# Kernel optimization log

Hardware: AMD Instinct MI355X
Metric: run time of the kernel (lower is better)

## Reference

```python
import jax, jax.numpy as jnp
import numpy as np

# dims
B, N, C_A, C_S, C_Z = 2, 8192, 128, 384, 16
H, D = 4, 32            # n_heads, head_dim (H*D == C_A)
NQ, NK = 32, 128        # local window: queries / keys
NB = 3                  # n_blocks
W = N // NQ             # number of query windows
HID = 2 * C_A           # transition expansion (n=2)


def _ln(x, eps=1e-5):
    # LayerNorm without affine params
    m = jnp.mean(x, axis=-1, keepdims=True)
    v = jnp.var(x, axis=-1, keepdims=True)
    return (x - m) * jax.lax.rsqrt(v + eps)


def setup_inputs() -> dict:
    key = jax.random.key(0)
    ks = iter(jax.random.split(key, 40))
    def rn(shape, scale=1.0):
        return jax.random.normal(next(ks), shape, dtype=jnp.float32) * jnp.float32(scale)
    inp = {
        'q': rn((B, N, C_A)),
        's': rn((B, N, C_S)),
        'p': rn((B, W, NQ, NK, C_Z)),
        # AttentionPairBias (AF3 Alg 24) params, stacked over blocks
        'adaln_scale_w': rn((NB, C_S, C_A), C_S ** -0.5),
        'adaln_scale_b': jnp.zeros((NB, C_A), jnp.float32),
        'adaln_shift_w': rn((NB, C_S, C_A), C_S ** -0.5),
        'wq': rn((NB, C_A, H * D), C_A ** -0.5),
        'bq': jnp.zeros((NB, H * D), jnp.float32),
        'wk': rn((NB, C_A, H * D), C_A ** -0.5),
        'wv': rn((NB, C_A, H * D), C_A ** -0.5),
        'lnz_w': jnp.ones((NB, C_Z), jnp.float32),
        'lnz_b': jnp.zeros((NB, C_Z), jnp.float32),
        'wb_pair': rn((NB, C_Z, H), C_Z ** -0.5),
        'wg': rn((NB, C_A, H * D), C_A ** -0.5),
        'wo': rn((NB, H * D, C_A), (H * D) ** -0.5),
        'sgate_w': rn((NB, C_S, C_A), C_S ** -0.5),
        'sgate_b': jnp.full((NB, C_A), -2.0, jnp.float32),
        # ConditionedTransitionBlock (AF3 Alg 25) params
        't_scale_w': rn((NB, C_S, C_A), C_S ** -0.5),
        't_scale_b': jnp.zeros((NB, C_A), jnp.float32),
        't_shift_w': rn((NB, C_S, C_A), C_S ** -0.5),
        't_wa': rn((NB, C_A, HID), C_A ** -0.5),
        't_wb': rn((NB, C_A, HID), C_A ** -0.5),
        't_wo': rn((NB, HID, C_A), HID ** -0.5),
        't_sgate_w': rn((NB, C_S, C_A), C_S ** -0.5),
        't_sgate_b': jnp.full((NB, C_A), -2.0, jnp.float32),
    }
    return inp


def reference(q, s, p,
              adaln_scale_w, adaln_scale_b, adaln_shift_w,
              wq, bq, wk, wv, lnz_w, lnz_b, wb_pair, wg, wo, sgate_w, sgate_b,
              t_scale_w, t_scale_b, t_shift_w, t_wa, t_wb, t_wo, t_sgate_w, t_sgate_b):
    a = q
    s_ln = _ln(s)  # [B, N, C_S], shared across blocks
    # local window key indices: window w covers queries [w*NQ, (w+1)*NQ), keys
    # are a centered NK-wide window -> offsets in [-(NK-NQ)//2, ...)
    off = (NK - NQ) // 2
    idx = jnp.arange(W)[:, None] * NQ - off + jnp.arange(NK)[None, :]  # [W, NK]
    valid = (idx >= 0) & (idx < N)
    idx_c = jnp.clip(idx, 0, N - 1)
    inv_sqrt_d = jnp.float32(1.0 / np.sqrt(D))
    NEG = jnp.float32(-1e9)

    for i in range(NB):
        # ---- AttentionPairBias (AdaLN-conditioned, pair-biased, gated) ----
        a_ln = _ln(a)
        a_ln = jax.nn.sigmoid(s_ln @ adaln_scale_w[i] + adaln_scale_b[i]) * a_ln \
               + s_ln @ adaln_shift_w[i]
        qh = (a_ln @ wq[i] + bq[i]).reshape(B, N, H, D)
        kh = (a_ln @ wk[i]).reshape(B, N, H, D)
        vh = (a_ln @ wv[i]).reshape(B, N, H, D)
        g = jax.nn.sigmoid(a_ln @ wg[i]).reshape(B, N, H, D)
        # pair bias from z: LN + linear to heads -> [B, W, NQ, NK, H]
        bias = (_ln(p) * lnz_w[i] + lnz_b[i]) @ wb_pair[i]
        qw = qh.reshape(B, W, NQ, H, D)
        kw = kh[:, idx_c]  # [B, W, NK, H, D]
        vw = vh[:, idx_c]
        logits = jnp.einsum('bwqhd,bwkhd->bwqkh', qw, kw) * inv_sqrt_d + bias
        logits = jnp.where(valid[None, :, None, :, None], logits, NEG)
        attn = jax.nn.softmax(logits, axis=3)
        ow = jnp.einsum('bwqkh,bwkhd->bwqhd', attn, vw)
        o = (g * ow.reshape(B, N, H, D)).reshape(B, N, H * D)
        attn_out = (o @ wo[i]) * jax.nn.sigmoid(s_ln @ sgate_w[i] + sgate_b[i])
        # ---- ConditionedTransitionBlock (SwiGLU, sigmoid-gated) ----
        t_ln = _ln(a)
        t_ln = jax.nn.sigmoid(s_ln @ t_scale_w[i] + t_scale_b[i]) * t_ln \
               + s_ln @ t_shift_w[i]
        hidden = jax.nn.silu(t_ln @ t_wa[i]) * (t_ln @ t_wb[i])
        trans_out = (hidden @ t_wo[i]) * jax.nn.sigmoid(s_ln @ t_sgate_w[i] + t_sgate_b[i])
        # AF3 Alg 23: a <- b + ConditionedTransitionBlock(a, s)
        a = attn_out + trans_out
    return a
```

## Files before the change

kernel.cpp:

```cpp
#include <hip/hip_runtime.h>
#include <hip/hip_bf16.h>
#include <cstddef>
#include <cstdint>

#define BB   2
#define NN   8192
#define CA   128
#define CS   384
#define CZ   16
#define HH   4
#define DD   32
#define NQW  32
#define NKW  128
#define NBLK 3
#define WW   256
#define MR   (BB*NN)
#define HIDN 256

typedef unsigned short u16;
typedef __attribute__((ext_vector_type(8))) short short8;
typedef __attribute__((ext_vector_type(4))) float floatx4;

__device__ __forceinline__ float sigmoidf_(float x) { return 1.f / (1.f + __expf(-x)); }

__device__ __forceinline__ u16 f2bf(float x) {
  unsigned u = __float_as_uint(x);
  unsigned r = (u + 0x7fffu + ((u >> 16) & 1u)) >> 16;
  return (u16)r;
}
__device__ __forceinline__ float bf2f(u16 u) {
  return __uint_as_float(((unsigned)u) << 16);
}

__device__ __forceinline__ void gload16(const u16* g, u16* l) {
  __builtin_amdgcn_global_load_lds(
      (const __attribute__((address_space(1))) unsigned int*)g,
      (__attribute__((address_space(3))) unsigned int*)l, 16, 0, 0);
}

__global__ __launch_bounds__(256) void ln_s_kernel(const float* __restrict__ s,
                                                   u16* __restrict__ s_ln_bf) {
  int row  = blockIdx.x * 4 + (threadIdx.x >> 6);
  int lane = threadIdx.x & 63;
  const float* sr = s + (size_t)row * CS;
  float x[6];
  float sum = 0.f, sq = 0.f;
#pragma unroll
  for (int t = 0; t < 6; ++t) { x[t] = sr[lane + 64*t]; sum += x[t]; sq += x[t]*x[t]; }
#pragma unroll
  for (int off = 32; off; off >>= 1) { sum += __shfl_down(sum, off); sq += __shfl_down(sq, off); }
  sum = __shfl(sum, 0); sq = __shfl(sq, 0);
  float mean = sum * (1.f/CS);
  float var  = sq  * (1.f/CS) - mean*mean;
  float rstd = rsqrtf(var + 1e-5f);
  u16* orow = s_ln_bf + (size_t)row * CS;
#pragma unroll
  for (int t = 0; t < 6; ++t) orow[lane + 64*t] = f2bf((x[t]-mean)*rstd);
}

__global__ __launch_bounds__(256) void modln_kernel(const float* __restrict__ a,
                                                    const u16* __restrict__ sp0,
                                                    const u16* __restrict__ sp1,
                                                    const u16* __restrict__ sp3,
                                                    const u16* __restrict__ sp4,
                                                    u16* __restrict__ amod,
                                                    u16* __restrict__ tmod) {
  int row  = blockIdx.x * 4 + (threadIdx.x >> 6);
  int lane = threadIdx.x & 63;
  const float* ar = a + (size_t)row * CA;
  float x0 = ar[lane], x1 = ar[lane + 64];
  float sum = x0 + x1, sq = x0*x0 + x1*x1;
#pragma unroll
  for (int off = 32; off; off >>= 1) { sum += __shfl_down(sum, off); sq += __shfl_down(sq, off); }
  sum = __shfl(sum, 0); sq = __shfl(sq, 0);
  float mean = sum * (1.f/CA);
  float var  = sq  * (1.f/CA) - mean*mean;
  float rstd = rsqrtf(var + 1e-5f);
  float n0 = (x0-mean)*rstd, n1 = (x1-mean)*rstd;
  size_t i0 = (size_t)row * CA + lane;
  amod[i0]      = f2bf(bf2f(sp0[i0])     *n0 + bf2f(sp1[i0]));
  amod[i0 + 64] = f2bf(bf2f(sp0[i0 + 64])*n1 + bf2f(sp1[i0 + 64]));
  tmod[i0]      = f2bf(bf2f(sp3[i0])     *n0 + bf2f(sp4[i0]));
  tmod[i0 + 64] = f2bf(bf2f(sp3[i0 + 64])*n1 + bf2f(sp4[i0 + 64]));
}

struct TJob { const float* src; u16* dst; int K; int N; };
struct TJobs { TJob j[42]; };

__global__ __launch_bounds__(256) void transpose_bf16(TJobs jobs) {
  TJob jb = jobs.j[blockIdx.z];
  int tk = blockIdx.x * 32, tn = blockIdx.y * 32;
  if (tk >= jb.K || tn >= jb.N) return;
  __shared__ float tile[32][33];
  int tx = threadIdx.x & 31;
  int ty = threadIdx.x >> 5;
#pragma unroll
  for (int r = ty; r < 32; r += 8) tile[r][tx] = jb.src[(size_t)(tk + r) * jb.N + tn + tx];
  __syncthreads();
#pragma unroll
  for (int r = ty; r < 32; r += 8)
    jb.dst[(size_t)(tn + r) * jb.K + tk + tx] = f2bf(tile[tx][r]);
}

struct GemmJob {
  const u16* A;
  const u16* Bt;
  const u16* Bt2;
  const float* bias;
  u16* outbf;
  int K;
  int ostride;
  int mode;
  int pad;
};
struct GemmJobs { GemmJob j[18]; };

template <int J, bool DUAL>
__global__ __launch_bounds__(256) void gemm_mfma(GemmJobs jobs) {
  const int jbase = blockIdx.z * J;
  const GemmJob jb0 = jobs.j[jbase];
  const int bm = blockIdx.y * 128, bn = blockIdx.x * 128;
  const int K = jb0.K;

  __shared__ u16 As[2][4096];
  __shared__ u16 Bs[2][J][4096];
  __shared__ u16 Bs2[DUAL ? 2 : 1][DUAL ? 4096 : 8];

  const int tid  = threadIdx.x;
  const int lane = tid & 63;
  const int wave = tid >> 6;
  const int wr = wave >> 1, wc = wave & 1;
  const int l15 = lane & 15, quad = lane >> 4;

  floatx4 acc[J][4][4] = {};
  floatx4 acc2[DUAL ? 4 : 1][DUAL ? 4 : 1] = {};

  const u16* Ab0 = jb0.A + ((size_t)bm + lane) * K + wave * 8;
  const u16* Ab1 = jb0.A + ((size_t)bm + 64 + lane) * K + wave * 8;
  const u16* Bb0[J];
  const u16* Bb1[J];
#pragma unroll
  for (int jj = 0; jj < J; ++jj) {
    const u16* Bt = jobs.j[jbase + jj].Bt;
    Bb0[jj] = Bt + ((size_t)bn + lane) * K + wave * 8;
    Bb1[jj] = Bt + ((size_t)bn + 64 + lane) * K + wave * 8;
  }
  const u16* B2b0 = DUAL ? (jb0.Bt2 + ((size_t)bn + lane) * K + wave * 8) : nullptr;
  const u16* B2b1 = DUAL ? (jb0.Bt2 + ((size_t)bn + 64 + lane) * K + wave * 8) : nullptr;

  auto stage = [&](int k0, int pb) {
    gload16(Ab0 + k0, As[pb] + wave * 1024);
    gload16(Ab1 + k0, As[pb] + wave * 1024 + 512);
#pragma unroll
    for (int jj = 0; jj < J; ++jj) {
      gload16(Bb0[jj] + k0, Bs[pb][jj] + wave * 1024);
      gload16(Bb1[jj] + k0, Bs[pb][jj] + wave * 1024 + 512);
    }
    if constexpr (DUAL) {
      gload16(B2b0 + k0, Bs2[pb] + wave * 1024);
      gload16(B2b1 + k0, Bs2[pb] + wave * 1024 + 512);
    }
  };

  stage(0, 0);
  __syncthreads();
  int cur = 0;
  for (int k0 = 0; k0 < K; k0 += 32) {
    if (k0 + 32 < K) stage(k0 + 32, cur ^ 1);

    short8 a_frag[4];
#pragma unroll
    for (int mt = 0; mt < 4; ++mt)
      a_frag[mt] = *(const short8*)(As[cur] + quad * 1024 + (wr * 64 + mt * 16 + l15) * 8);
#pragma unroll
    for (int jj = 0; jj < J; ++jj) {
      short8 b_frag[4];
#pragma unroll
      for (int nt = 0; nt < 4; ++nt)
        b_frag[nt] = *(const short8*)(Bs[cur][jj] + quad * 1024 + (wc * 64 + nt * 16 + l15) * 8);
#pragma unroll
      for (int mt = 0; mt < 4; ++mt)
#pragma unroll
        for (int nt = 0; nt < 4; ++nt)
          acc[jj][mt][nt] = __builtin_amdgcn_mfma_f32_16x16x32_bf16(a_frag[mt], b_frag[nt], acc[jj][mt][nt], 0, 0, 0);
    }
    if constexpr (DUAL) {
      short8 b2_frag[4];
#pragma unroll
      for (int nt = 0; nt < 4; ++nt)
        b2_frag[nt] = *(const short8*)(Bs2[cur] + quad * 1024 + (wc * 64 + nt * 16 + l15) * 8);
#pragma unroll
      for (int mt = 0; mt < 4; ++mt)
#pragma unroll
        for (int nt = 0; nt < 4; ++nt)
          acc2[mt][nt] = __builtin_amdgcn_mfma_f32_16x16x32_bf16(a_frag[mt], b2_frag[nt], acc2[mt][nt], 0, 0, 0);
    }
    __syncthreads();
    cur ^= 1;
  }

#pragma unroll
  for (int jj = 0; jj < J; ++jj) {
    GemmJob jb = jobs.j[jbase + jj];
#pragma unroll
    for (int mt = 0; mt < 4; ++mt) {
#pragma unroll
      for (int nt = 0; nt < 4; ++nt) {
        int n = bn + wc * 64 + nt * 16 + l15;
        int mbase = bm + wr * 64 + mt * 16 + quad * 4;
        floatx4 v = acc[jj][mt][nt];
        if constexpr (DUAL) {
          floatx4 v2 = acc2[mt][nt];
#pragma unroll
          for (int r = 0; r < 4; ++r) {
            size_t idx = (size_t)(mbase + r) * jb.ostride + n;
            float x1 = v[r];
            jb.outbf[idx] = f2bf(x1 * sigmoidf_(x1) * v2[r]);
          }
        } else if (jb.mode == 5) {
          int bidx = mbase >> 13;
          int tok  = mbase & (NN - 1);
          ushort4 o;
          o.x = f2bf(v[0]); o.y = f2bf(v[1]); o.z = f2bf(v[2]); o.w = f2bf(v[3]);
          *(ushort4*)(jb.outbf + (size_t)(bidx * CA + n) * NN + tok) = o;
        } else {
          float bias = jb.bias ? jb.bias[n] : 0.f;
#pragma unroll
          for (int r = 0; r < 4; ++r) {
            size_t idx = (size_t)(mbase + r) * jb.ostride + n;
            float x = v[r] + bias;
            jb.outbf[idx] = f2bf(jb.mode == 1 ? sigmoidf_(x) : x);
          }
        }
      }
    }
  }
}

__global__ __launch_bounds__(256) void combo_kernel(const u16* __restrict__ O,
                                                    const u16* __restrict__ HID,
                                                    const u16* __restrict__ woT,
                                                    const u16* __restrict__ twoT,
                                                    const u16* __restrict__ g1,
                                                    const u16* __restrict__ g2,
                                                    float* __restrict__ outp) {
  const int bm = blockIdx.y * 64;
  __shared__ u16 As1[2][2048];
  __shared__ u16 Bs1[2][4096];
  __shared__ u16 As2[2][2048];
  __shared__ u16 Bs2h[2][4096];
  const int tid  = threadIdx.x;
  const int lane = tid & 63;
  const int wave = tid >> 6;
  const int wr = wave >> 1, wc = wave & 1;
  const int l15 = lane & 15, quad = lane >> 4;

  floatx4 acc1[2][4] = {};
  floatx4 acc2[2][4] = {};

  const u16* A1  = O    + ((size_t)bm + lane) * CA + wave * 8;
  const u16* B10 = woT  + ((size_t)lane) * CA + wave * 8;
  const u16* B11 = woT  + ((size_t)64 + lane) * CA + wave * 8;
  const u16* A2  = HID  + ((size_t)bm + lane) * HIDN + wave * 8;
  const u16* B20 = twoT + ((size_t)lane) * HIDN + wave * 8;
  const u16* B21 = twoT + ((size_t)64 + lane) * HIDN + wave * 8;

  auto stage1 = [&](int k0, int pb) {
    gload16(A1  + k0, As1[pb] + wave * 512);
    gload16(B10 + k0, Bs1[pb] + wave * 1024);
    gload16(B11 + k0, Bs1[pb] + wave * 1024 + 512);
  };
  auto stage2 = [&](int k0, int pb) {
    gload16(A2  + k0, As2[pb] + wave * 512);
    gload16(B20 + k0, Bs2h[pb] + wave * 1024);
    gload16(B21 + k0, Bs2h[pb] + wave * 1024 + 512);
  };

  stage1(0, 0);
  stage2(0, 0);
  __syncthreads();
  int cur = 0;
  for (int t = 0; t < 8; ++t) {
    if (t + 1 < 4) stage1((t + 1) * 32, cur ^ 1);
    if (t + 1 < 8) stage2((t + 1) * 32, cur ^ 1);

    if (t < 4) {
      short8 a_frag[2], b_frag[4];
#pragma unroll
      for (int mt = 0; mt < 2; ++mt)
        a_frag[mt] = *(const short8*)(As1[cur] + quad * 512 + (wr * 32 + mt * 16 + l15) * 8);
#pragma unroll
      for (int nt = 0; nt < 4; ++nt)
        b_frag[nt] = *(const short8*)(Bs1[cur] + quad * 1024 + (wc * 64 + nt * 16 + l15) * 8);
#pragma unroll
      for (int mt = 0; mt < 2; ++mt)
#pragma unroll
        for (int nt = 0; nt < 4; ++nt)
          acc1[mt][nt] = __builtin_amdgcn_mfma_f32_16x16x32_bf16(a_frag[mt], b_frag[nt], acc1[mt][nt], 0, 0, 0);
    }
    {
      short8 a_frag[2], b_frag[4];
#pragma unroll
      for (int mt = 0; mt < 2; ++mt)
        a_frag[mt] = *(const short8*)(As2[cur] + quad * 512 + (wr * 32 + mt * 16 + l15) * 8);
#pragma unroll
      for (int nt = 0; nt < 4; ++nt)
        b_frag[nt] = *(const short8*)(Bs2h[cur] + quad * 1024 + (wc * 64 + nt * 16 + l15) * 8);
#pragma unroll
      for (int mt = 0; mt < 2; ++mt)
#pragma unroll
        for (int nt = 0; nt < 4; ++nt)
          acc2[mt][nt] = __builtin_amdgcn_mfma_f32_16x16x32_bf16(a_frag[mt], b_frag[nt], acc2[mt][nt], 0, 0, 0);
    }
    __syncthreads();
    cur ^= 1;
  }

#pragma unroll
  for (int mt = 0; mt < 2; ++mt) {
#pragma unroll
    for (int nt = 0; nt < 4; ++nt) {
      int n = wc * 64 + nt * 16 + l15;
      int mbase = bm + wr * 32 + mt * 16 + quad * 4;
#pragma unroll
      for (int r = 0; r < 4; ++r) {
        size_t idx = (size_t)(mbase + r) * CA + n;
        outp[idx] = acc1[mt][nt][r] * bf2f(g1[idx]) + acc2[mt][nt][r] * bf2f(g2[idx]);
      }
    }
  }
}

__global__ __launch_bounds__(256) void bias3_kernel(const float* __restrict__ p,
                                                    const float* __restrict__ lnz_w,
                                                    const float* __restrict__ lnz_b,
                                                    const float* __restrict__ wb,
                                                    u16* __restrict__ biasT) {
  const int kc = blockIdx.x, w = blockIdx.y, b = blockIdx.z;
  __shared__ float effW[12][16];
  __shared__ float effb[12];
  const int t = threadIdx.x;
  if (t < 192) {
    int i = t >> 6, rem = t & 63, z = rem >> 2, hh = rem & 3;
    effW[i*4 + hh][z] = lnz_w[i*CZ + z] * wb[(i*CZ + z)*HH + hh];
  }
  if (t < 12) {
    int i = t >> 2, hh = t & 3;
    float acc = 0.f;
    for (int z = 0; z < 16; ++z) acc += lnz_b[i*CZ + z] * wb[(i*CZ + z)*HH + hh];
    effb[t] = acc;
  }
  __syncthreads();

  const int kk = t & 31, qg = (t >> 5) * 4;
  const int k = kc * 32 + kk;
  u16 out4[12][4];
#pragma unroll
  for (int r = 0; r < 4; ++r) {
    int qq = qg + r;
    const float4* pr = (const float4*)(p + (size_t)(((b * WW + w) * NQW + qq) * NKW + k) * 16);
    float4 p0 = pr[0], p1 = pr[1], p2 = pr[2], p3 = pr[3];
    float x[16] = {p0.x,p0.y,p0.z,p0.w, p1.x,p1.y,p1.z,p1.w,
                   p2.x,p2.y,p2.z,p2.w, p3.x,p3.y,p3.z,p3.w};
    float sum = 0.f, sq = 0.f;
#pragma unroll
    for (int z = 0; z < 16; ++z) { sum += x[z]; sq += x[z]*x[z]; }
    float mean = sum * (1.f/16.f);
    float var  = sq  * (1.f/16.f) - mean*mean;
    float rstd = rsqrtf(var + 1e-5f);
#pragma unroll
    for (int ih = 0; ih < 12; ++ih) {
      float acc = effb[ih];
#pragma unroll
      for (int z = 0; z < 16; ++z) acc += (x[z]-mean)*rstd * effW[ih][z];
      out4[ih][r] = f2bf(acc);
    }
  }
#pragma unroll
  for (int ih = 0; ih < 12; ++ih) {
    int i = ih >> 2, hh = ih & 3;
    u16* dst = biasT + ((((size_t)i * BB + b) * WW + w) * HH + hh) * 4096 + (size_t)k * 32 + qg;
    ushort4 uv; uv.x = out4[ih][0]; uv.y = out4[ih][1]; uv.z = out4[ih][2]; uv.w = out4[ih][3];
    *(ushort4*)dst = uv;
  }
}

__global__ __launch_bounds__(64) void attn_mfma(const u16* __restrict__ Qb,
                                                const u16* __restrict__ Kb,
                                                const u16* __restrict__ Vtb,
                                                const u16* __restrict__ Gb,
                                                const u16* __restrict__ biasT,
                                                u16* __restrict__ Ob) {
  const int w = blockIdx.x, h = blockIdx.y, b = blockIdx.z;
  __shared__ u16 Pt[128 * 36];
  __shared__ float inv_s[32];
  const int lane = threadIdx.x;
  const int l15 = lane & 15, quad = lane >> 4;
  const int tok0 = w * NQW - 48;

  short8 qf[2];
#pragma unroll
  for (int mt = 0; mt < 2; ++mt) {
    int qq = w * NQW + mt * 16 + l15;
    qf[mt] = *(const short8*)(Qb + (size_t)(b * NN + qq) * CA + h * DD + quad * 8);
  }
  floatx4 lg[2][8] = {};
#pragma unroll
  for (int nt = 0; nt < 8; ++nt) {
    int tk = tok0 + nt * 16 + l15;
    int tc = min(max(tk, 0), NN - 1);
    short8 kf = *(const short8*)(Kb + (size_t)(b * NN + tc) * CA + h * DD + quad * 8);
#pragma unroll
    for (int mt = 0; mt < 2; ++mt)
      lg[mt][nt] = __builtin_amdgcn_mfma_f32_16x16x32_bf16(qf[mt], kf, lg[mt][nt], 0, 0, 0);
  }

  const float scale = 0.17677669529663687f;
  const u16* bb = biasT + ((((size_t)b * WW + w) * HH + h) << 12);
  float mrow[2][4];
#pragma unroll
  for (int mt = 0; mt < 2; ++mt)
#pragma unroll
    for (int r = 0; r < 4; ++r) mrow[mt][r] = -3.0e38f;
#pragma unroll
  for (int nt = 0; nt < 8; ++nt) {
    int tk = tok0 + nt * 16 + l15;
    bool valid = (tk >= 0) && (tk < NN);
#pragma unroll
    for (int mt = 0; mt < 2; ++mt) {
      ushort4 bv = *(const ushort4*)(bb + (nt * 16 + l15) * 32 + mt * 16 + quad * 4);
      float bvf[4] = {bf2f(bv.x), bf2f(bv.y), bf2f(bv.z), bf2f(bv.w)};
#pragma unroll
      for (int r = 0; r < 4; ++r) {
        float l = valid ? (lg[mt][nt][r] * scale + bvf[r]) : -1e9f;
        lg[mt][nt][r] = l;
        mrow[mt][r] = fmaxf(mrow[mt][r], l);
      }
    }
  }
#pragma unroll
  for (int mt = 0; mt < 2; ++mt)
#pragma unroll
    for (int r = 0; r < 4; ++r) {
      float m = mrow[mt][r];
      m = fmaxf(m, __shfl_xor(m, 1));
      m = fmaxf(m, __shfl_xor(m, 2));
      m = fmaxf(m, __shfl_xor(m, 4));
      m = fmaxf(m, __shfl_xor(m, 8));
      mrow[mt][r] = m;
    }

  float srow[2][4] = {};
#pragma unroll
  for (int nt = 0; nt < 8; ++nt)
#pragma unroll
    for (int mt = 0; mt < 2; ++mt) {
      u16 pv[4];
#pragma unroll
      for (int r = 0; r < 4; ++r) {
        float e = __expf(lg[mt][nt][r] - mrow[mt][r]);
        srow[mt][r] += e;
        pv[r] = f2bf(e);
      }
      ushort4 uv; uv.x = pv[0]; uv.y = pv[1]; uv.z = pv[2]; uv.w = pv[3];
      *(ushort4*)(Pt + (nt * 16 + l15) * 36 + mt * 16 + quad * 4) = uv;
    }
#pragma unroll
  for (int mt = 0; mt < 2; ++mt)
#pragma unroll
    for (int r = 0; r < 4; ++r) {
      float ssum = srow[mt][r];
      ssum += __shfl_xor(ssum, 1);
      ssum += __shfl_xor(ssum, 2);
      ssum += __shfl_xor(ssum, 4);
      ssum += __shfl_xor(ssum, 8);
      if (l15 == 0) inv_s[mt * 16 + quad * 4 + r] = 1.f / ssum;
    }
  __syncthreads();

  floatx4 oacc[2][2] = {};
#pragma unroll
  for (int ks = 0; ks < 4; ++ks) {
    short8 pf[2];
#pragma unroll
    for (int ntq = 0; ntq < 2; ++ntq)
#pragma unroll
      for (int j = 0; j < 8; ++j)
        pf[ntq][j] = (short)Pt[(ks * 32 + quad * 8 + j) * 36 + ntq * 16 + l15];
    int tb = tok0 + ks * 32 + quad * 8;
    tb = min(max(tb, 0), NN - 8);
#pragma unroll
    for (int mtd = 0; mtd < 2; ++mtd) {
      short8 vf = *(const short8*)(Vtb + (size_t)(b * CA + h * DD + mtd * 16 + l15) * NN + tb);
#pragma unroll
      for (int ntq = 0; ntq < 2; ++ntq)
        oacc[mtd][ntq] = __builtin_amdgcn_mfma_f32_16x16x32_bf16(vf, pf[ntq], oacc[mtd][ntq], 0, 0, 0);
    }
  }

#pragma unroll
  for (int mtd = 0; mtd < 2; ++mtd)
#pragma unroll
    for (int ntq = 0; ntq < 2; ++ntq) {
      int qq = ntq * 16 + l15;
      float inv = inv_s[qq];
      int tok = w * NQW + qq;
      size_t base = (size_t)(b * NN + tok) * CA + h * DD + mtd * 16 + quad * 4;
      ushort4 gv = *(const ushort4*)(Gb + base);
      floatx4 v = oacc[mtd][ntq];
      ushort4 o;
      o.x = f2bf(bf2f(gv.x) * v[0] * inv);
      o.y = f2bf(bf2f(gv.y) * v[1] * inv);
      o.z = f2bf(bf2f(gv.z) * v[2] * inv);
      o.w = f2bf(bf2f(gv.w) * v[3] * inv);
      *(ushort4*)(Ob + base) = o;
    }
}

extern "C" void kernel_launch(void* const* d_in, const int* in_sizes, int n_in,
                              void* d_out, int out_size, void* d_ws, size_t ws_size,
                              hipStream_t stream) {
  const float* q             = (const float*)d_in[0];
  const float* s             = (const float*)d_in[1];
  const float* p             = (const float*)d_in[2];
  const float* adaln_scale_w = (const float*)d_in[3];
  const float* adaln_scale_b = (const float*)d_in[4];
  const float* adaln_shift_w = (const float*)d_in[5];
  const float* wq            = (const float*)d_in[6];
  const float* bq            = (const float*)d_in[7];
  const float* wk            = (const float*)d_in[8];
  const float* wv            = (const float*)d_in[9];
  const float* lnz_w         = (const float*)d_in[10];
  const float* lnz_b         = (const float*)d_in[11];
  const float* wb_pair       = (const float*)d_in[12];
  const float* wg            = (const float*)d_in[13];
  const float* wo            = (const float*)d_in[14];
  const float* sgate_w       = (const float*)d_in[15];
  const float* sgate_b       = (const float*)d_in[16];
  const float* t_scale_w     = (const float*)d_in[17];
  const float* t_scale_b     = (const float*)d_in[18];
  const float* t_shift_w     = (const float*)d_in[19];
  const float* t_wa          = (const float*)d_in[20];
  const float* t_wb          = (const float*)d_in[21];
  const float* t_wo          = (const float*)d_in[22];
  const float* t_sgate_w     = (const float*)d_in[23];
  const float* t_sgate_b     = (const float*)d_in[24];
  float* out = (float*)d_out;

  const size_t MC = (size_t)MR * CA;
  float* fws   = (float*)d_ws;
  float* abuf0 = fws;
  float* abuf1 = abuf0 + MC;
  u16* uws     = (u16*)(abuf1 + MC);
  u16* s_ln_bf = uws;
  u16* SP      = s_ln_bf + (size_t)MR * CS;
  u16* amod    = SP + 18*MC;
  u16* tmod    = amod + MC;
  u16* Qb      = tmod + MC;
  u16* Kb      = Qb + MC;
  u16* Vtb     = Kb + MC;
  u16* Gb      = Vtb + MC;
  u16* Ob      = Gb + MC;
  u16* HIDb    = Ob + MC;
  u16* biasT   = HIDb + 2*MC;
  u16* wbuf    = biasT + (size_t)3*BB*WW*HH*NQW*NKW;

  const size_t WBLK = 6*(size_t)CA*CS + 5*(size_t)CA*CA + 3*(size_t)CA*HIDN;
  const size_t o_ascale = 0;
  const size_t o_ashift = o_ascale + (size_t)CA*CS;
  const size_t o_sgate  = o_ashift + (size_t)CA*CS;
  const size_t o_tscale = o_sgate  + (size_t)CA*CS;
  const size_t o_tshift = o_tscale + (size_t)CA*CS;
  const size_t o_tsgate = o_tshift + (size_t)CA*CS;
  const size_t o_wq     = o_tsgate + (size_t)CA*CS;
  const size_t o_wk     = o_wq + (size_t)CA*CA;
  const size_t o_wv     = o_wk + (size_t)CA*CA;
  const size_t o_wg     = o_wv + (size_t)CA*CA;
  const size_t o_wo     = o_wg + (size_t)CA*CA;
  const size_t o_twa    = o_wo + (size_t)CA*CA;
  const size_t o_twb    = o_twa + (size_t)HIDN*CA;
  const size_t o_two    = o_twb + (size_t)HIDN*CA;

  ln_s_kernel<<<MR/4, 256, 0, stream>>>(s, s_ln_bf);

  TJobs tj;
  for (int i = 0; i < NBLK; ++i) {
    u16* wb0 = wbuf + (size_t)i * WBLK;
    int b14 = i * 14;
    tj.j[b14+0]  = TJob{adaln_scale_w + (size_t)i*CS*CA, wb0 + o_ascale, CS, CA};
    tj.j[b14+1]  = TJob{adaln_shift_w + (size_t)i*CS*CA, wb0 + o_ashift, CS, CA};
    tj.j[b14+2]  = TJob{sgate_w       + (size_t)i*CS*CA, wb0 + o_sgate,  CS, CA};
    tj.j[b14+3]  = TJob{t_scale_w     + (size_t)i*CS*CA, wb0 + o_tscale, CS, CA};
    tj.j[b14+4]  = TJob{t_shift_w     + (size_t)i*CS*CA, wb0 + o_tshift, CS, CA};
    tj.j[b14+5]  = TJob{t_sgate_w     + (size_t)i*CS*CA, wb0 + o_tsgate, CS, CA};
    tj.j[b14+6]  = TJob{wq   + (size_t)i*CA*CA,   wb0 + o_wq,  CA, CA};
    tj.j[b14+7]  = TJob{wk   + (size_t)i*CA*CA,   wb0 + o_wk,  CA, CA};
    tj.j[b14+8]  = TJob{wv   + (size_t)i*CA*CA,   wb0 + o_wv,  CA, CA};
    tj.j[b14+9]  = TJob{wg   + (size_t)i*CA*CA,   wb0 + o_wg,  CA, CA};
    tj.j[b14+10] = TJob{wo   + (size_t)i*CA*CA,   wb0 + o_wo,  CA, CA};
    tj.j[b14+11] = TJob{t_wa + (size_t)i*CA*HIDN, wb0 + o_twa, CA, HIDN};
    tj.j[b14+12] = TJob{t_wb + (size_t)i*CA*HIDN, wb0 + o_twb, CA, HIDN};
    tj.j[b14+13] = TJob{t_wo + (size_t)i*HIDN*CA, wb0 + o_two, HIDN, CA};
  }
  transpose_bf16<<<dim3(12, 8, 42), 256, 0, stream>>>(tj);

  bias3_kernel<<<dim3(4, WW, BB), 256, 0, stream>>>(p, lnz_w, lnz_b, wb_pair, biasT);

  {
    GemmJobs js = {};
    for (int i = 0; i < NBLK; ++i) {
      u16* wb0 = wbuf + (size_t)i * WBLK;
      js.j[i*6+0] = GemmJob{s_ln_bf, wb0 + o_ascale, nullptr, adaln_scale_b + i*CA, SP + (i*6+0)*MC, CS, CA, 1, 0};
      js.j[i*6+1] = GemmJob{s_ln_bf, wb0 + o_ashift, nullptr, nullptr,              SP + (i*6+1)*MC, CS, CA, 0, 0};
      js.j[i*6+2] = GemmJob{s_ln_bf, wb0 + o_sgate,  nullptr, sgate_b   + i*CA,     SP + (i*6+2)*MC, CS, CA, 1, 0};
      js.j[i*6+3] = GemmJob{s_ln_bf, wb0 + o_tscale, nullptr, t_scale_b + i*CA,     SP + (i*6+3)*MC, CS, CA, 1, 0};
      js.j[i*6+4] = GemmJob{s_ln_bf, wb0 + o_tshift, nullptr, nullptr,              SP + (i*6+4)*MC, CS, CA, 0, 0};
      js.j[i*6+5] = GemmJob{s_ln_bf, wb0 + o_tsgate, nullptr, t_sgate_b + i*CA,     SP + (i*6+5)*MC, CS, CA, 1, 0};
    }
    gemm_mfma<3, false><<<dim3(1, MR/128, 6), 256, 0, stream>>>(js);
  }

  for (int i = 0; i < NBLK; ++i) {
    const float* a_in = (i == 0) ? q : (i == 1 ? abuf0 : abuf1);
    float* a_out = (i == 2) ? out : (i == 0 ? abuf0 : abuf1);
    u16* wb0 = wbuf + (size_t)i * WBLK;

    modln_kernel<<<MR/4, 256, 0, stream>>>(a_in, SP + (i*6+0)*MC, SP + (i*6+1)*MC,
                                           SP + (i*6+3)*MC, SP + (i*6+4)*MC, amod, tmod);

    GemmJobs jq = {};
    jq.j[0] = GemmJob{amod, wb0 + o_wq, nullptr, bq + i*CA, Qb,  CA, CA, 0, 0};
    jq.j[1] = GemmJob{amod, wb0 + o_wk, nullptr, nullptr,   Kb,  CA, CA, 0, 0};
    jq.j[2] = GemmJob{amod, wb0 + o_wv, nullptr, nullptr,   Vtb, CA, CA, 5, 0};
    jq.j[3] = GemmJob{amod, wb0 + o_wg, nullptr, nullptr,   Gb,  CA, CA, 1, 0};
    gemm_mfma<2, false><<<dim3(1, MR/128, 2), 256, 0, stream>>>(jq);

    GemmJobs jh = {};
    jh.j[0] = GemmJob{tmod, wb0 + o_twa, wb0 + o_twb, nullptr, HIDb, CA, HIDN, 4, 0};
    gemm_mfma<1, true><<<dim3(2, MR/128, 1), 256, 0, stream>>>(jh);

    attn_mfma<<<dim3(WW, HH, BB), 64, 0, stream>>>(
        Qb, Kb, Vtb, Gb, biasT + (size_t)i * BB*WW*HH*4096, Ob);

    combo_kernel<<<dim3(1, MR/64), 256, 0, stream>>>(
        Ob, HIDb, wb0 + o_wo, wb0 + o_two,
        SP + (i*6+2)*MC, SP + (i*6+5)*MC, a_out);
  }
}
```

Before: 637.8 us.

## Flatten multi-job GEMM to one job per workgroup with XCD-aware swizzled grid

The batched GEMM kernel no longer processes several weight matrices per workgroup sharing one A tile. Each workgroup now computes a single job's 128x128 tile, and the flat 1D grid index is swizzled in groups of 8 so that consecutive tiles of the same rows land on the same XCD. This trades A-tile reuse across jobs for more workgroups, a smaller accumulator and LDS footprint (better occupancy), and L2 locality across chiplets. The cost is more global and L2 reads of A.

After: 576.9 us. 1.11x faster.

```diff
diff --git a/kernel.cpp b/kernel.cpp
--- a/kernel.cpp
+++ b/kernel.cpp
@@ -115,15 +115,21 @@
 };
 struct GemmJobs { GemmJob j[18]; };
 
-template <int J, bool DUAL>
+template <int NJ, int NX, bool DUAL>
 __global__ __launch_bounds__(256) void gemm_mfma(GemmJobs jobs) {
-  const int jbase = blockIdx.z * J;
-  const GemmJob jb0 = jobs.j[jbase];
-  const int bm = blockIdx.y * 128, bn = blockIdx.x * 128;
-  const int K = jb0.K;
+  constexpr int NWG = NJ * NX * (MR / 128);
+  const int lin = blockIdx.x;
+  const int swz = (lin & 7) * (NWG >> 3) + (lin >> 3);
+  const int job  = swz % NJ;
+  const int rest = swz / NJ;
+  const int bn = (rest % NX) * 128;
+  const int bm = (rest / NX) * 128;
+
+  GemmJob jb = jobs.j[job];
+  const int K = jb.K;
 
   __shared__ u16 As[2][4096];
-  __shared__ u16 Bs[2][J][4096];
+  __shared__ u16 Bs[2][4096];
   __shared__ u16 Bs2[DUAL ? 2 : 1][DUAL ? 4096 : 8];
 
   const int tid  = threadIdx.x;
@@ -132,30 +138,21 @@
   const int wr = wave >> 1, wc = wave & 1;
   const int l15 = lane & 15, quad = lane >> 4;
 
-  floatx4 acc[J][4][4] = {};
+  floatx4 acc[4][4] = {};
   floatx4 acc2[DUAL ? 4 : 1][DUAL ? 4 : 1] = {};
 
-  const u16* Ab0 = jb0.A + ((size_t)bm + lane) * K + wave * 8;
-  const u16* Ab1 = jb0.A + ((size_t)bm + 64 + lane) * K + wave * 8;
-  const u16* Bb0[J];
-  const u16* Bb1[J];
-#pragma unroll
-  for (int jj = 0; jj < J; ++jj) {
-    const u16* Bt = jobs.j[jbase + jj].Bt;
-    Bb0[jj] = Bt + ((size_t)bn + lane) * K + wave * 8;
-    Bb1[jj] = Bt + ((size_t)bn + 64 + lane) * K + wave * 8;
-  }
-  const u16* B2b0 = DUAL ? (jb0.Bt2 + ((size_t)bn + lane) * K + wave * 8) : nullptr;
-  const u16* B2b1 = DUAL ? (jb0.Bt2 + ((size_t)bn + 64 + lane) * K + wave * 8) : nullptr;
+  const u16* Ab0  = jb.A  + ((size_t)bm + lane) * K + wave * 8;
+  const u16* Ab1  = jb.A  + ((size_t)bm + 64 + lane) * K + wave * 8;
+  const u16* Bb0  = jb.Bt + ((size_t)bn + lane) * K + wave * 8;
+  const u16* Bb1  = jb.Bt + ((size_t)bn + 64 + lane) * K + wave * 8;
+  const u16* B2b0 = DUAL ? (jb.Bt2 + ((size_t)bn + lane) * K + wave * 8) : nullptr;
+  const u16* B2b1 = DUAL ? (jb.Bt2 + ((size_t)bn + 64 + lane) * K + wave * 8) : nullptr;
 
   auto stage = [&](int k0, int pb) {
     gload16(Ab0 + k0, As[pb] + wave * 1024);
     gload16(Ab1 + k0, As[pb] + wave * 1024 + 512);
-#pragma unroll
-    for (int jj = 0; jj < J; ++jj) {
-      gload16(Bb0[jj] + k0, Bs[pb][jj] + wave * 1024);
-      gload16(Bb1[jj] + k0, Bs[pb][jj] + wave * 1024 + 512);
-    }
+    gload16(Bb0 + k0, Bs[pb] + wave * 1024);
+    gload16(Bb1 + k0, Bs[pb] + wave * 1024 + 512);
     if constexpr (DUAL) {
       gload16(B2b0 + k0, Bs2[pb] + wave * 1024);
       gload16(B2b1 + k0, Bs2[pb] + wave * 1024 + 512);
@@ -168,22 +165,18 @@
   for (int k0 = 0; k0 < K; k0 += 32) {
     if (k0 + 32 < K) stage(k0 + 32, cur ^ 1);
 
-    short8 a_frag[4];
+    short8 a_frag[4], b_frag[4];
 #pragma unroll
     for (int mt = 0; mt < 4; ++mt)
       a_frag[mt] = *(const short8*)(As[cur] + quad * 1024 + (wr * 64 + mt * 16 + l15) * 8);
 #pragma unroll
-    for (int jj = 0; jj < J; ++jj) {
-      short8 b_frag[4];
+    for (int nt = 0; nt < 4; ++nt)
+      b_frag[nt] = *(const short8*)(Bs[cur] + quad * 1024 + (wc * 64 + nt * 16 + l15) * 8);
+#pragma unroll
+    for (int mt = 0; mt < 4; ++mt)
 #pragma unroll
       for (int nt = 0; nt < 4; ++nt)
-        b_frag[nt] = *(const short8*)(Bs[cur][jj] + quad * 1024 + (wc * 64 + nt * 16 + l15) * 8);
-#pragma unroll
-      for (int mt = 0; mt < 4; ++mt)
-#pragma unroll
-        for (int nt = 0; nt < 4; ++nt)
-          acc[jj][mt][nt] = __builtin_amdgcn_mfma_f32_16x16x32_bf16(a_frag[mt], b_frag[nt], acc[jj][mt][nt], 0, 0, 0);
-    }
+        acc[mt][nt] = __builtin_amdgcn_mfma_f32_16x16x32_bf16(a_frag[mt], b_frag[nt], acc[mt][nt], 0, 0, 0);
     if constexpr (DUAL) {
       short8 b2_frag[4];
 #pragma unroll
@@ -200,37 +193,33 @@
   }
 
 #pragma unroll
-  for (int jj = 0; jj < J; ++jj) {
-    GemmJob jb = jobs.j[jbase + jj];
-#pragma unroll
-    for (int mt = 0; mt < 4; ++mt) {
-#pragma unroll
-      for (int nt = 0; nt < 4; ++nt) {
-        int n = bn + wc * 64 + nt * 16 + l15;
-        int mbase = bm + wr * 64 + mt * 16 + quad * 4;
-        floatx4 v = acc[jj][mt][nt];
-        if constexpr (DUAL) {
-          floatx4 v2 = acc2[mt][nt];
-#pragma unroll
-          for (int r = 0; r < 4; ++r) {
-            size_t idx = (size_t)(mbase + r) * jb.ostride + n;
-            float x1 = v[r];
-            jb.outbf[idx] = f2bf(x1 * sigmoidf_(x1) * v2[r]);
-          }
-        } else if (jb.mode == 5) {
-          int bidx = mbase >> 13;
-          int tok  = mbase & (NN - 1);
-          ushort4 o;
-          o.x = f2bf(v[0]); o.y = f2bf(v[1]); o.z = f2bf(v[2]); o.w = f2bf(v[3]);
-          *(ushort4*)(jb.outbf + (size_t)(bidx * CA + n) * NN + tok) = o;
-        } else {
-          float bias = jb.bias ? jb.bias[n] : 0.f;
-#pragma unroll
-          for (int r = 0; r < 4; ++r) {
-            size_t idx = (size_t)(mbase + r) * jb.ostride + n;
-            float x = v[r] + bias;
-            jb.outbf[idx] = f2bf(jb.mode == 1 ? sigmoidf_(x) : x);
-          }
+  for (int mt = 0; mt < 4; ++mt) {
+#pragma unroll
+    for (int nt = 0; nt < 4; ++nt) {
+      int n = bn + wc * 64 + nt * 16 + l15;
+      int mbase = bm + wr * 64 + mt * 16 + quad * 4;
+      floatx4 v = acc[mt][nt];
+      if constexpr (DUAL) {
+        floatx4 v2 = acc2[mt][nt];
+#pragma unroll
+        for (int r = 0; r < 4; ++r) {
+          size_t idx = (size_t)(mbase + r) * jb.ostride + n;
+          float x1 = v[r];
+          jb.outbf[idx] = f2bf(x1 * sigmoidf_(x1) * v2[r]);
+        }
+      } else if (jb.mode == 5) {
+        int bidx = mbase >> 13;
+        int tok  = mbase & (NN - 1);
+        ushort4 o;
+        o.x = f2bf(v[0]); o.y = f2bf(v[1]); o.z = f2bf(v[2]); o.w = f2bf(v[3]);
+        *(ushort4*)(jb.outbf + (size_t)(bidx * CA + n) * NN + tok) = o;
+      } else {
+        float bias = jb.bias ? jb.bias[n] : 0.f;
+#pragma unroll
+        for (int r = 0; r < 4; ++r) {
+          size_t idx = (size_t)(mbase + r) * jb.ostride + n;
+          float x = v[r] + bias;
+          jb.outbf[idx] = f2bf(jb.mode == 1 ? sigmoidf_(x) : x);
         }
       }
     }
@@ -617,7 +606,7 @@
       js.j[i*6+4] = GemmJob{s_ln_bf, wb0 + o_tshift, nullptr, nullptr,              SP + (i*6+4)*MC, CS, CA, 0, 0};
       js.j[i*6+5] = GemmJob{s_ln_bf, wb0 + o_tsgate, nullptr, t_sgate_b + i*CA,     SP + (i*6+5)*MC, CS, CA, 1, 0};
     }
-    gemm_mfma<3, false><<<dim3(1, MR/128, 6), 256, 0, stream>>>(js);
+    gemm_mfma<18, 1, false><<<18 * (MR/128), 256, 0, stream>>>(js);
   }
 
   for (int i = 0; i < NBLK; ++i) {
@@ -633,11 +622,11 @@
     jq.j[1] = GemmJob{amod, wb0 + o_wk, nullptr, nullptr,   Kb,  CA, CA, 0, 0};
     jq.j[2] = GemmJob{amod, wb0 + o_wv, nullptr, nullptr,   Vtb, CA, CA, 5, 0};
     jq.j[3] = GemmJob{amod, wb0 + o_wg, nullptr, nullptr,   Gb,  CA, CA, 1, 0};
-    gemm_mfma<2, false><<<dim3(1, MR/128, 2), 256, 0, stream>>>(jq);
+    gemm_mfma<4, 1, false><<<4 * (MR/128), 256, 0, stream>>>(jq);
 
     GemmJobs jh = {};
     jh.j[0] = GemmJob{tmod, wb0 + o_twa, wb0 + o_twb, nullptr, HIDb, CA, HIDN, 4, 0};
-    gemm_mfma<1, true><<<dim3(2, MR/128, 1), 256, 0, stream>>>(jh);
+    gemm_mfma<1, 2, true><<<2 * (MR/128), 256, 0, stream>>>(jh);
 
     attn_mfma<<<dim3(WW, HH, BB), 64, 0, stream>>>(
         Qb, Kb, Vtb, Gb, biasT + (size_t)i * BB*WW*HH*4096, Ob);
```
